# Kernel tuning notes

Hardware: AMD Instinct MI355X
Metric: run time of the kernel (lower is better)

## Reference

```python
import jax, jax.numpy as jnp
import numpy as np

N, E, IN, H, OUT = 100000, 1600000, 128, 128, 64


def setup_inputs() -> dict:
    key = jax.random.key(0)
    ks = jax.random.split(key, 7)
    x = jax.random.normal(ks[0], (N, IN), dtype=jnp.float32)
    edge_index = jax.random.randint(ks[1], (2, E), 0, N, dtype=jnp.int32)
    # Glorot-style scaled params (PyG SAGEConv: lin_l has bias, lin_r does not)
    s1 = 1.0 / np.sqrt(IN)
    s2 = 1.0 / np.sqrt(H)
    W1_l = jax.random.normal(ks[2], (H, IN), dtype=jnp.float32) * s1
    W1_r = jax.random.normal(ks[3], (H, IN), dtype=jnp.float32) * s1
    b1 = jnp.zeros((H,), dtype=jnp.float32)
    W2_l = jax.random.normal(ks[4], (OUT, H), dtype=jnp.float32) * s2
    W2_r = jax.random.normal(ks[5], (OUT, H), dtype=jnp.float32) * s2
    b2 = jnp.zeros((OUT,), dtype=jnp.float32)
    return {"x": x, "W1_l": W1_l, "W1_r": W1_r, "b1": b1,
            "W2_l": W2_l, "W2_r": W2_r, "b2": b2, "edge_index": edge_index}


def _sage_conv(x, edge_index, W_l, W_r, b):
    # mean-aggregate source-node features at target nodes, then linear + root term
    src, dst = edge_index[0], edge_index[1]
    n = x.shape[0]
    msgs = x[src]                                                   # [E, d]
    agg = jax.ops.segment_sum(msgs, dst, num_segments=n)            # [N, d]
    deg = jax.ops.segment_sum(jnp.ones((src.shape[0],), x.dtype), dst, num_segments=n)
    mean = agg / jnp.clip(deg, 1.0)[:, None]                        # zero-deg nodes stay 0
    return mean @ W_l.T + b + x @ W_r.T


def reference(x, W1_l, W1_r, b1, W2_l, W2_r, b2, edge_index):
    h = _sage_conv(x, edge_index, W1_l, W1_r, b1)
    h = jax.nn.relu(h)  # dropout p=0.0 -> identity
    out = _sage_conv(h, edge_index, W2_l, W2_r, b2)
    return out
```

## Files before the change

kernel.cpp:

```cpp
#include <hip/hip_runtime.h>


typedef unsigned int uint32;
typedef short bf16x8 __attribute__((ext_vector_type(8)));
typedef float f32x16 __attribute__((ext_vector_type(16)));
typedef float f32x2 __attribute__((ext_vector_type(2)));

#define PSTR 264

__device__ __forceinline__ uint32 pack_bf16_rne(float a, float b) {
    uint32 ua = __float_as_uint(a);
    uint32 ub = __float_as_uint(b);
    uint32 ra = (ua + 0x7fffu + ((ua >> 16) & 1u)) >> 16;
    uint32 rb = (ub + 0x7fffu + ((ub >> 16) & 1u)) >> 16;
    return ra | (rb << 16);
}
__device__ __forceinline__ float bf_lo(uint32 v) { return __uint_as_float(v << 16); }
__device__ __forceinline__ float bf_hi(uint32 v) { return __uint_as_float(v & 0xffff0000u); }

__device__ __forceinline__ short rne16(float v, float* back) {
    uint32 u = __float_as_uint(v);
    uint32 r = (u + 0x7fffu + ((u >> 16) & 1u)) >> 16;
    *back = __uint_as_float(r << 16);
    return (short)r;
}

__global__ void k_prep(const float* __restrict__ x, uint32* __restrict__ xb,
                       long n4,
                       const float* __restrict__ W1l, const float* __restrict__ W1r,
                       const float* __restrict__ W2l, const float* __restrict__ W2r,
                       short* __restrict__ W1pH, short* __restrict__ W1pL,
                       short* __restrict__ W2pH, short* __restrict__ W2pL) {
    long i = (long)blockIdx.x * blockDim.x + threadIdx.x;
    float back;
    if (i < n4) {
        float4 v = ((const float4*)x)[i];
        short h0 = rne16(v.x, &back);
        short h1 = rne16(v.y, &back);
        short h2 = rne16(v.z, &back);
        short h3 = rne16(v.w, &back);
        uint2 o;
        o.x = (uint32)(unsigned short)h0 | ((uint32)(unsigned short)h1 << 16);
        o.y = (uint32)(unsigned short)h2 | ((uint32)(unsigned short)h3 << 16);
        ((uint2*)xb)[i] = o;
        return;
    }
    int i2 = (int)(i - n4);
    if (i2 < 32768) {
        int j = i2 >> 8, k = i2 & 255;
        float v = (k < 128) ? W1l[j * 128 + k] : W1r[j * 128 + k - 128];
        float hb;
        short hs = rne16(v, &hb);
        short ls = rne16(v - hb, &back);
        int idx = (k >> 3) * 1024 + j * 8 + (k & 7);
        W1pH[idx] = hs;
        W1pL[idx] = ls;
    } else if (i2 < 32768 + 16384) {
        int i3 = i2 - 32768;
        int j = i3 >> 7, k = i3 & 127;
        float v = (j < 64) ? W2l[j * 128 + k] : W2r[(j - 64) * 128 + k];
        float hb;
        short hs = rne16(v, &hb);
        short ls = rne16(v - hb, &back);
        int idx = (k >> 3) * 1024 + j * 8 + (k & 7);
        W2pH[idx] = hs;
        W2pL[idx] = ls;
    }
}


__global__ void k_bcount(const int* __restrict__ ei, int E, int NB,
                         int* __restrict__ bucket_cnt) {
    __shared__ int hist[1024];
    int t = threadIdx.x;
    for (int i = t; i < NB; i += 256) hist[i] = 0;
    __syncthreads();
    int stride = gridDim.x * 256;
    for (int e = blockIdx.x * 256 + t; e < E; e += stride)
        atomicAdd(&hist[ei[E + e] >> 8], 1);
    __syncthreads();
    for (int i = t; i < NB; i += 256) {
        int c = hist[i];
        if (c) atomicAdd(&bucket_cnt[i], c);
    }
}

__global__ void k_bscan(const int* __restrict__ bucket_cnt, int NB, int E,
                        int* __restrict__ bucket_off, int* __restrict__ bucket_cur) {
    __shared__ int s[1024];
    int t = threadIdx.x;
    int v = (t < NB) ? bucket_cnt[t] : 0;
    s[t] = v;
    __syncthreads();
    for (int o = 1; o < 1024; o <<= 1) {
        int u = (t >= o) ? s[t - o] : 0;
        __syncthreads();
        s[t] += u;
        __syncthreads();
    }
    int ex = s[t] - v;
    if (t < NB) { bucket_off[t] = ex; bucket_cur[t] = ex; }
    if (t == NB - 1) bucket_off[NB] = ex + v;
}

__global__ void k_bscatter(const int* __restrict__ ei, int E, int NB,
                           int* __restrict__ bucket_cur, uint32* __restrict__ eb) {
    __shared__ int hist[1024];
    __shared__ int base[1024];
    int t = threadIdx.x;
    for (int i = t; i < NB; i += 256) hist[i] = 0;
    __syncthreads();
    int stride = gridDim.x * 256;
    for (int e = blockIdx.x * 256 + t; e < E; e += stride)
        atomicAdd(&hist[ei[E + e] >> 8], 1);
    __syncthreads();
    for (int i = t; i < NB; i += 256) {
        int c = hist[i];
        base[i] = c ? atomicAdd(&bucket_cur[i], c) : 0;
        hist[i] = 0;
    }
    __syncthreads();
    for (int e = blockIdx.x * 256 + t; e < E; e += stride) {
        int d = ei[E + e];
        int b = d >> 8;
        int r = atomicAdd(&hist[b], 1);
        eb[base[b] + r] = ((uint32)(d & 255) << 24) | (uint32)ei[e];
    }
}

__global__ void k_bfinal(const uint32* __restrict__ eb,
                         const int* __restrict__ bucket_off,
                         int* __restrict__ row_ptr, int* __restrict__ col,
                         int N, int E) {
    __shared__ int deg[256];
    __shared__ int sc[256];
    __shared__ int cur[256];
    int b = blockIdx.x;
    int t = threadIdx.x;
    int beg = bucket_off[b], end = bucket_off[b + 1];
    deg[t] = 0;
    __syncthreads();
    for (int e = beg + t; e < end; e += 256)
        atomicAdd(&deg[eb[e] >> 24], 1);
    __syncthreads();
    int v = deg[t];
    sc[t] = v;
    __syncthreads();
    for (int o = 1; o < 256; o <<= 1) {
        int u = (t >= o) ? sc[t - o] : 0;
        __syncthreads();
        sc[t] += u;
        __syncthreads();
    }
    int ex = sc[t] - v;
    int node = b * 256 + t;
    if (node < N) row_ptr[node] = beg + ex;
    if (b == gridDim.x - 1 && t == 0) row_ptr[N] = E;
    cur[t] = ex;
    __syncthreads();
    for (int e = beg + t; e < end; e += 256) {
        uint32 u = eb[e];
        int r = atomicAdd(&cur[u >> 24], 1);
        col[beg + r] = (int)(u & 0xFFFFFFu);
    }
}


__global__ __launch_bounds__(256, 4) void k_fused(
        const int* __restrict__ rp, const int* __restrict__ col,
        const uint32* __restrict__ xb,
        const short* __restrict__ W1pH, const short* __restrict__ W1pL,
        const short* __restrict__ W2pH, const short* __restrict__ W2pL,
        const float* __restrict__ b1, const float* __restrict__ b2,
        unsigned short* __restrict__ hl, float* __restrict__ hr, int N) {
    __shared__ short smH[16 * PSTR];
    __shared__ short smL[16 * PSTR];
    int t = threadIdx.x;
    int w = t >> 6, lane = t & 63;
    int node0 = blockIdx.x * 32;

    int base = node0 + 8 * w;
    int rpi = base + lane;
    if (rpi > N) rpi = N;
    int rpv = rp[rpi];

#define ACC1(a) { s += (f32x2){bf_lo(a), __uint_as_float(a)}; }

    for (int i = 0; i < 8; i++) {
        int lr = 8 * w + i;
        int beg = __builtin_amdgcn_readfirstlane(__shfl(rpv, i));
        int end = __builtin_amdgcn_readfirstlane(__shfl(rpv, i + 1));
        f32x2 s = (f32x2){0.f, 0.f};
        int e = beg;
        for (; e + 8 <= end; e += 8) {
            int c0 = col[e + 0], c1 = col[e + 1], c2 = col[e + 2], c3 = col[e + 3];
            int c4 = col[e + 4], c5 = col[e + 5], c6 = col[e + 6], c7 = col[e + 7];
            uint32 a0 = xb[(size_t)c0 * 64 + lane];
            uint32 a1 = xb[(size_t)c1 * 64 + lane];
            uint32 a2 = xb[(size_t)c2 * 64 + lane];
            uint32 a3 = xb[(size_t)c3 * 64 + lane];
            uint32 a4 = xb[(size_t)c4 * 64 + lane];
            uint32 a5 = xb[(size_t)c5 * 64 + lane];
            uint32 a6 = xb[(size_t)c6 * 64 + lane];
            uint32 a7 = xb[(size_t)c7 * 64 + lane];
            ACC1(a0); ACC1(a1); ACC1(a2); ACC1(a3);
            ACC1(a4); ACC1(a5); ACC1(a6); ACC1(a7);
        }
        for (; e + 4 <= end; e += 4) {
            int c0 = col[e + 0], c1 = col[e + 1], c2 = col[e + 2], c3 = col[e + 3];
            uint32 a0 = xb[(size_t)c0 * 64 + lane];
            uint32 a1 = xb[(size_t)c1 * 64 + lane];
            uint32 a2 = xb[(size_t)c2 * 64 + lane];
            uint32 a3 = xb[(size_t)c3 * 64 + lane];
            ACC1(a0); ACC1(a1); ACC1(a2); ACC1(a3);
        }
        for (; e < end; e++) {
            uint32 a0 = xb[(size_t)col[e] * 64 + lane];
            ACC1(a0);
        }
        float inv = 1.0f / (float)max(end - beg, 1);
        float m0 = s.x * inv, m1 = s.y * inv;
        float b_;
        short h0 = rne16(m0, &b_);
        float bk0 = b_;
        short l0 = rne16(m0 - bk0, &b_);
        short h1 = rne16(m1, &b_);
        float bk1 = b_;
        short l1 = rne16(m1 - bk1, &b_);
        uint32 H = (uint32)(unsigned short)h0 | ((uint32)(unsigned short)h1 << 16);
        uint32 L = (uint32)(unsigned short)l0 | ((uint32)(unsigned short)l1 << 16);
        int idx = (lane >> 2) * PSTR + lr * 8 + 2 * (lane & 3);
        *(uint32*)&smH[idx] = H;
        *(uint32*)&smL[idx] = L;
    }
#undef ACC1
    __syncthreads();

    int m = lane & 31, hh = lane >> 5;
    int mynode = node0 + m;
    const short* xbs = (const short*)xb;
    f32x16 acc;
#pragma unroll
    for (int r = 0; r < 16; r++) acc[r] = 0.f;
#pragma unroll
    for (int kc = 0; kc < 8; kc++) {
        int c = 2 * kc + hh;
        bf16x8 bH = *(const bf16x8*)&smH[c * PSTR + m * 8];
        bf16x8 bL = *(const bf16x8*)&smL[c * PSTR + m * 8];
        bf16x8 xH = *(const bf16x8*)(xbs + (size_t)mynode * 128 + c * 8);
        bf16x8 aH1 = *(const bf16x8*)(W1pH + c * 1024 + (32 * w + m) * 8);
        bf16x8 aL1 = *(const bf16x8*)(W1pL + c * 1024 + (32 * w + m) * 8);
        bf16x8 aH2 = *(const bf16x8*)(W1pH + (16 + c) * 1024 + (32 * w + m) * 8);
        bf16x8 aL2 = *(const bf16x8*)(W1pL + (16 + c) * 1024 + (32 * w + m) * 8);
        acc = __builtin_amdgcn_mfma_f32_32x32x16_bf16(aH1, bH, acc, 0, 0, 0);
        acc = __builtin_amdgcn_mfma_f32_32x32x16_bf16(aL1, bH, acc, 0, 0, 0);
        acc = __builtin_amdgcn_mfma_f32_32x32x16_bf16(aH1, bL, acc, 0, 0, 0);
        acc = __builtin_amdgcn_mfma_f32_32x32x16_bf16(aH2, xH, acc, 0, 0, 0);
        acc = __builtin_amdgcn_mfma_f32_32x32x16_bf16(aL2, xH, acc, 0, 0, 0);
    }

    uint2 oh[4], ol[4];
#pragma unroll
    for (int rg = 0; rg < 4; rg++) {
        int j0 = 32 * w + 8 * rg + 4 * hh;
        float4 bv = *(const float4*)(b1 + j0);
        float bb[4] = {bv.x, bv.y, bv.z, bv.w};
        short hs[4], ls[4];
#pragma unroll
        for (int q = 0; q < 4; q++) {
            float v = fmaxf(acc[4 * rg + q] + bb[q], 0.f);
            float back;
            hs[q] = rne16(v, &back);
            ls[q] = rne16(v - back, &back);
        }
        oh[rg].x = (uint32)(unsigned short)hs[0] | ((uint32)(unsigned short)hs[1] << 16);
        oh[rg].y = (uint32)(unsigned short)hs[2] | ((uint32)(unsigned short)hs[3] << 16);
        ol[rg].x = (uint32)(unsigned short)ls[0] | ((uint32)(unsigned short)ls[1] << 16);
        ol[rg].y = (uint32)(unsigned short)ls[2] | ((uint32)(unsigned short)ls[3] << 16);
    }
    __syncthreads();
#pragma unroll
    for (int rg = 0; rg < 4; rg++) {
        int idx = (4 * w + rg) * PSTR + m * 8 + 4 * hh;
        *(uint2*)&smH[idx] = oh[rg];
        *(uint2*)&smL[idx] = ol[rg];
    }
    __syncthreads();

#pragma unroll
    for (int r = 0; r < 16; r++) acc[r] = 0.f;
#pragma unroll
    for (int kc = 0; kc < 8; kc++) {
        int c = 2 * kc + hh;
        bf16x8 bH = *(const bf16x8*)&smH[c * PSTR + m * 8];
        bf16x8 bL = *(const bf16x8*)&smL[c * PSTR + m * 8];
        bf16x8 aH = *(const bf16x8*)(W2pH + c * 1024 + (32 * w + m) * 8);
        bf16x8 aL = *(const bf16x8*)(W2pL + c * 1024 + (32 * w + m) * 8);
        acc = __builtin_amdgcn_mfma_f32_32x32x16_bf16(aH, bH, acc, 0, 0, 0);
        acc = __builtin_amdgcn_mfma_f32_32x32x16_bf16(aL, bH, acc, 0, 0, 0);
        acc = __builtin_amdgcn_mfma_f32_32x32x16_bf16(aH, bL, acc, 0, 0, 0);
    }
    if (mynode >= N) return;
    if (w < 2) {
#pragma unroll
        for (int rg = 0; rg < 4; rg++) {
            int j0 = 32 * w + 8 * rg + 4 * hh;
            uint2 o;
            o.x = pack_bf16_rne(acc[4 * rg + 0], acc[4 * rg + 1]);
            o.y = pack_bf16_rne(acc[4 * rg + 2], acc[4 * rg + 3]);
            *(uint2*)&hl[(size_t)mynode * 64 + j0] = o;
        }
    } else {
#pragma unroll
        for (int rg = 0; rg < 4; rg++) {
            int j0 = 32 * (w - 2) + 8 * rg + 4 * hh;
            float4 bv = *(const float4*)(b2 + j0);
            float4 o;
            o.x = acc[4 * rg + 0] + bv.x;
            o.y = acc[4 * rg + 1] + bv.y;
            o.z = acc[4 * rg + 2] + bv.z;
            o.w = acc[4 * rg + 3] + bv.w;
            *(float4*)&hr[(size_t)mynode * 64 + j0] = o;
        }
    }
}


__global__ void k_agg_out(const int* __restrict__ rp, const int* __restrict__ col,
                          const unsigned short* __restrict__ hl,
                          const float* __restrict__ hr,
                          float* __restrict__ out, int N) {
    int node = blockIdx.x * 8 + (threadIdx.x >> 5);
    if (node >= N) return;
    int h = threadIdx.x & 31;
    int g = h >> 3;
    int f = h & 7;
    int beg = rp[node], end = rp[node + 1];
    const uint4* hl4 = (const uint4*)hl;
    f32x2 sA[4];
#pragma unroll
    for (int j = 0; j < 4; j++) sA[j] = (f32x2){0.f, 0.f};

#define ACC_MSK(v)                                          \
    { sA[0] += (f32x2){bf_lo(v.x), bf_hi(v.x)};             \
      sA[1] += (f32x2){bf_lo(v.y), bf_hi(v.y)};             \
      sA[2] += (f32x2){bf_lo(v.z), bf_hi(v.z)};             \
      sA[3] += (f32x2){bf_lo(v.w), bf_hi(v.w)}; }

    int e = beg;
    for (; e + 16 <= end; e += 16) {
        uint4 cv = *(const uint4*)(col + e + 4 * g);
        uint4 v0 = hl4[(size_t)cv.x * 8 + f];
        uint4 v1 = hl4[(size_t)cv.y * 8 + f];
        uint4 v2 = hl4[(size_t)cv.z * 8 + f];
        uint4 v3 = hl4[(size_t)cv.w * 8 + f];
        ACC_MSK(v0); ACC_MSK(v1); ACC_MSK(v2); ACC_MSK(v3);
    }
    for (; e + 8 <= end; e += 8) {
        uint2 cv = *(const uint2*)(col + e + 2 * g);
        uint4 v0 = hl4[(size_t)cv.x * 8 + f];
        uint4 v1 = hl4[(size_t)cv.y * 8 + f];
        ACC_MSK(v0); ACC_MSK(v1);
    }
    int rem = end - e;
    if (2 * g < rem) {
        uint4 v0 = hl4[(size_t)col[e + 2 * g] * 8 + f];
        ACC_MSK(v0);
    }
    if (2 * g + 1 < rem) {
        uint4 v0 = hl4[(size_t)col[e + 2 * g + 1] * 8 + f];
        ACC_MSK(v0);
    }
#undef ACC_MSK
#pragma unroll
    for (int p = 0; p < 4; p++) {
        sA[p].x += __shfl_xor(sA[p].x, 8);
        sA[p].y += __shfl_xor(sA[p].y, 8);
        sA[p].x += __shfl_xor(sA[p].x, 16);
        sA[p].y += __shfl_xor(sA[p].y, 16);
    }
    if (g == 0) {
        float inv = 1.0f / (float)max(end - beg, 1);
        const float* hrp = hr + (size_t)node * 64 + f * 8;
        float4 h0 = *(const float4*)(hrp);
        float4 h1 = *(const float4*)(hrp + 4);
        float4 o0, o1;
        o0.x = sA[0].x * inv + h0.x;
        o0.y = sA[0].y * inv + h0.y;
        o0.z = sA[1].x * inv + h0.z;
        o0.w = sA[1].y * inv + h0.w;
        o1.x = sA[2].x * inv + h1.x;
        o1.y = sA[2].y * inv + h1.y;
        o1.z = sA[3].x * inv + h1.z;
        o1.w = sA[3].y * inv + h1.w;
        float* op = out + (size_t)node * 64 + f * 8;
        *(float4*)(op) = o0;
        *(float4*)(op + 4) = o1;
    }
}

extern "C" void kernel_launch(void* const* d_in, const int* in_sizes, int n_in,
                              void* d_out, int out_size, void* d_ws, size_t ws_size,
                              hipStream_t stream) {
    const float* x   = (const float*)d_in[0];
    const float* W1l = (const float*)d_in[1];
    const float* W1r = (const float*)d_in[2];
    const float* b1  = (const float*)d_in[3];
    const float* W2l = (const float*)d_in[4];
    const float* W2r = (const float*)d_in[5];
    const float* b2  = (const float*)d_in[6];
    const int*   ei  = (const int*)d_in[7];
    int N = in_sizes[0] / 128;
    int E = in_sizes[7] / 2;
    int NB = (N + 255) >> 8;
    int mb = (N + 31) / 32;
    int Np = ((N + 127) / 128) * 128;
    float* out = (float*)d_out;

    char* w = (char*)d_ws;
    size_t off = 0;
    auto alloc = [&](size_t bytes) -> char* {
        char* p = w + off;
        off += (bytes + 255) & ~(size_t)255;
        return p;
    };
    int*   row_ptr = (int*)alloc((size_t)(N + 1) * 4);
    int*   bcnt    = (int*)alloc((size_t)(NB + 1) * 4);
    int*   boff    = (int*)alloc((size_t)(NB + 1) * 4);
    int*   bcur    = (int*)alloc((size_t)(NB + 1) * 4);
    short* W1pH    = (short*)alloc(32768 * 2);
    short* W1pL    = (short*)alloc(32768 * 2);
    short* W2pH    = (short*)alloc(16384 * 2);
    short* W2pL    = (short*)alloc(16384 * 2);
    int*   col     = (int*)alloc((size_t)E * 4);
    uint32* xb     = (uint32*)alloc((size_t)Np * 64 * 4);
    float*  hr     = (float*)alloc((size_t)Np * 64 * 4);
    unsigned short* hl = (unsigned short*)alloc((size_t)N * 64 * 2);
    uint32* eb = (uint32*)hl;

    hipMemsetAsync(bcnt, 0, (size_t)NB * 4, stream);
    long n4 = (long)N * 32;
    long prep_items = n4 + 32768 + 16384;
    k_prep<<<(int)((prep_items + 255) / 256), 256, 0, stream>>>(
        x, xb, n4, W1l, W1r, W2l, W2r, W1pH, W1pL, W2pH, W2pL);
    k_bcount<<<256, 256, 0, stream>>>(ei, E, NB, bcnt);
    k_bscan<<<1, 1024, 0, stream>>>(bcnt, NB, E, boff, bcur);
    k_bscatter<<<128, 256, 0, stream>>>(ei, E, NB, bcur, eb);
    k_bfinal<<<NB, 256, 0, stream>>>(eb, boff, row_ptr, col, N, E);

    k_fused<<<mb, 256, 0, stream>>>(row_ptr, col, xb, W1pH, W1pL, W2pH, W2pL,
                                    b1, b2, hl, hr, N);
    int ab = (N + 7) / 8;
    k_agg_out<<<ab, 256, 0, stream>>>(row_ptr, col, hl, hr, out, N);
}
```

Measured before the change: 314.8 us.

## Replace two-level bucketed CSR build with direct global-atomic counting sort

Replaces the four-kernel bucketed CSR construction (bucket histogram, bucket scan, bucket scatter, per-bucket local sort) with three kernels: per-node degree counting via global atomics, a single-block scan over all N degrees, and a scatter using global atomic cursors. This removes one kernel launch and the intermediate packed edge buffer pass, at the cost of heavier global atomic traffic and a single-block scan over 100k entries. Edge order within each row becomes nondeterministic, which changes floating-point summation order.

Result: slower. 494.3 us (+57.0%).

```diff
diff --git a/kernel.cpp b/kernel.cpp
--- a/kernel.cpp
+++ b/kernel.cpp
@@ -69,99 +69,66 @@
 }
 
 
-__global__ void k_bcount(const int* __restrict__ ei, int E, int NB,
-                         int* __restrict__ bucket_cnt) {
-    __shared__ int hist[1024];
+__global__ void k_deg(const int* __restrict__ ei, int E, int* __restrict__ deg) {
+    int stride = gridDim.x * 256;
+    for (int e = blockIdx.x * 256 + threadIdx.x; e < E; e += stride)
+        atomicAdd(&deg[ei[E + e]], 1);
+}
+
+__global__ void k_scan(const int* __restrict__ deg, int* __restrict__ rp,
+                       int* __restrict__ cur, int N, int E) {
+    __shared__ int part[1024];
     int t = threadIdx.x;
-    for (int i = t; i < NB; i += 256) hist[i] = 0;
-    __syncthreads();
-    int stride = gridDim.x * 256;
-    for (int e = blockIdx.x * 256 + t; e < E; e += stride)
-        atomicAdd(&hist[ei[E + e] >> 8], 1);
-    __syncthreads();
-    for (int i = t; i < NB; i += 256) {
-        int c = hist[i];
-        if (c) atomicAdd(&bucket_cnt[i], c);
-    }
-}
-
-__global__ void k_bscan(const int* __restrict__ bucket_cnt, int NB, int E,
-                        int* __restrict__ bucket_off, int* __restrict__ bucket_cur) {
-    __shared__ int s[1024];
-    int t = threadIdx.x;
-    int v = (t < NB) ? bucket_cnt[t] : 0;
-    s[t] = v;
+    int chunk = (((N + 1023) >> 10) + 3) & ~3;
+    int beg = t * chunk;
+    int end = min(beg + chunk, N);
+    int s = 0;
+    for (int i = beg; i < end; i += 4) {
+        if (i + 4 <= end) {
+            int4 v = *(const int4*)(deg + i);
+            s += v.x + v.y + v.z + v.w;
+        } else {
+            for (int j = i; j < end; j++) s += deg[j];
+        }
+    }
+    part[t] = s;
     __syncthreads();
     for (int o = 1; o < 1024; o <<= 1) {
-        int u = (t >= o) ? s[t - o] : 0;
+        int u = (t >= o) ? part[t - o] : 0;
         __syncthreads();
-        s[t] += u;
+        part[t] += u;
         __syncthreads();
     }
-    int ex = s[t] - v;
-    if (t < NB) { bucket_off[t] = ex; bucket_cur[t] = ex; }
-    if (t == NB - 1) bucket_off[NB] = ex + v;
-}
-
-__global__ void k_bscatter(const int* __restrict__ ei, int E, int NB,
-                           int* __restrict__ bucket_cur, uint32* __restrict__ eb) {
-    __shared__ int hist[1024];
-    __shared__ int base[1024];
-    int t = threadIdx.x;
-    for (int i = t; i < NB; i += 256) hist[i] = 0;
-    __syncthreads();
+    int run = part[t] - s;
+    for (int i = beg; i < end; i += 4) {
+        if (i + 4 <= end) {
+            int4 v = *(const int4*)(deg + i);
+            int4 o;
+            o.x = run; run += v.x;
+            o.y = run; run += v.y;
+            o.z = run; run += v.z;
+            o.w = run; run += v.w;
+            *(int4*)(rp + i) = o;
+            *(int4*)(cur + i) = o;
+        } else {
+            for (int j = i; j < end; j++) {
+                rp[j] = run;
+                cur[j] = run;
+                run += deg[j];
+            }
+        }
+    }
+    if (t == 0) rp[N] = E;
+}
+
+__global__ void k_scatter(const int* __restrict__ ei, int E,
+                          int* __restrict__ cur, int* __restrict__ col) {
     int stride = gridDim.x * 256;
-    for (int e = blockIdx.x * 256 + t; e < E; e += stride)
-        atomicAdd(&hist[ei[E + e] >> 8], 1);
-    __syncthreads();
-    for (int i = t; i < NB; i += 256) {
-        int c = hist[i];
-        base[i] = c ? atomicAdd(&bucket_cur[i], c) : 0;
-        hist[i] = 0;
-    }
-    __syncthreads();
-    for (int e = blockIdx.x * 256 + t; e < E; e += stride) {
+    for (int e = blockIdx.x * 256 + threadIdx.x; e < E; e += stride) {
         int d = ei[E + e];
-        int b = d >> 8;
-        int r = atomicAdd(&hist[b], 1);
-        eb[base[b] + r] = ((uint32)(d & 255) << 24) | (uint32)ei[e];
-    }
-}
-
-__global__ void k_bfinal(const uint32* __restrict__ eb,
-                         const int* __restrict__ bucket_off,
-                         int* __restrict__ row_ptr, int* __restrict__ col,
-                         int N, int E) {
-    __shared__ int deg[256];
-    __shared__ int sc[256];
-    __shared__ int cur[256];
-    int b = blockIdx.x;
-    int t = threadIdx.x;
-    int beg = bucket_off[b], end = bucket_off[b + 1];
-    deg[t] = 0;
-    __syncthreads();
-    for (int e = beg + t; e < end; e += 256)
-        atomicAdd(&deg[eb[e] >> 24], 1);
-    __syncthreads();
-    int v = deg[t];
-    sc[t] = v;
-    __syncthreads();
-    for (int o = 1; o < 256; o <<= 1) {
-        int u = (t >= o) ? sc[t - o] : 0;
-        __syncthreads();
-        sc[t] += u;
-        __syncthreads();
-    }
-    int ex = sc[t] - v;
-    int node = b * 256 + t;
-    if (node < N) row_ptr[node] = beg + ex;
-    if (b == gridDim.x - 1 && t == 0) row_ptr[N] = E;
-    cur[t] = ex;
-    __syncthreads();
-    for (int e = beg + t; e < end; e += 256) {
-        uint32 u = eb[e];
-        int r = atomicAdd(&cur[u >> 24], 1);
-        col[beg + r] = (int)(u & 0xFFFFFFu);
+        int s = ei[e];
+        int r = atomicAdd(&cur[d], 1);
+        col[r] = s;
     }
 }
 
@@ -412,7 +379,6 @@
     const int*   ei  = (const int*)d_in[7];
     int N = in_sizes[0] / 128;
     int E = in_sizes[7] / 2;
-    int NB = (N + 255) >> 8;
     int mb = (N + 31) / 32;
     int Np = ((N + 127) / 128) * 128;
     float* out = (float*)d_out;
@@ -425,9 +391,8 @@
         return p;
     };
     int*   row_ptr = (int*)alloc((size_t)(N + 1) * 4);
-    int*   bcnt    = (int*)alloc((size_t)(NB + 1) * 4);
-    int*   boff    = (int*)alloc((size_t)(NB + 1) * 4);
-    int*   bcur    = (int*)alloc((size_t)(NB + 1) * 4);
+    int*   deg     = (int*)alloc((size_t)(N + 1) * 4);
+    int*   cur     = (int*)alloc((size_t)(N + 1) * 4);
     short* W1pH    = (short*)alloc(32768 * 2);
     short* W1pL    = (short*)alloc(32768 * 2);
     short* W2pH    = (short*)alloc(16384 * 2);
@@ -436,17 +401,15 @@
     uint32* xb     = (uint32*)alloc((size_t)Np * 64 * 4);
     float*  hr     = (float*)alloc((size_t)Np * 64 * 4);
     unsigned short* hl = (unsigned short*)alloc((size_t)N * 64 * 2);
-    uint32* eb = (uint32*)hl;
-
-    hipMemsetAsync(bcnt, 0, (size_t)NB * 4, stream);
+
+    hipMemsetAsync(deg, 0, (size_t)N * 4, stream);
     long n4 = (long)N * 32;
     long prep_items = n4 + 32768 + 16384;
     k_prep<<<(int)((prep_items + 255) / 256), 256, 0, stream>>>(
         x, xb, n4, W1l, W1r, W2l, W2r, W1pH, W1pL, W2pH, W2pL);
-    k_bcount<<<256, 256, 0, stream>>>(ei, E, NB, bcnt);
-    k_bscan<<<1, 1024, 0, stream>>>(bcnt, NB, E, boff, bcur);
-    k_bscatter<<<128, 256, 0, stream>>>(ei, E, NB, bcur, eb);
-    k_bfinal<<<NB, 256, 0, stream>>>(eb, boff, row_ptr, col, N, E);
+    k_deg<<<2048, 256, 0, stream>>>(ei, E, deg);
+    k_scan<<<1, 1024, 0, stream>>>(deg, row_ptr, cur, N, E);
+    k_scatter<<<2048, 256, 0, stream>>>(ei, E, cur, col);
 
     k_fused<<<mb, 256, 0, stream>>>(row_ptr, col, xb, W1pH, W1pL, W2pH, W2pL,
                                     b1, b2, hl, hr, N);
```
